# Performance work log

Measured on AMD Instinct MI355X. Metric: run time of the kernel, lower is better.

## Reference

```python
import jax, jax.numpy as jnp
import numpy as np

N_NODES = 100000
N_EDGES = 1600000
IN_F = 256
OUT_F = 64


def setup_inputs() -> dict:
    key = jax.random.key(0)
    k1, k2, k3, k4, k5, k6 = jax.random.split(key, 6)
    x = jax.random.normal(k1, (N_NODES, IN_F), dtype=jnp.float32)
    edge_vals = jax.random.uniform(k2, (N_EDGES,), dtype=jnp.float32)
    W = jax.random.normal(k3, (IN_F, OUT_F), dtype=jnp.float32) * (1.0 / np.sqrt(OUT_F))
    bias = jax.random.normal(k4, (OUT_F,), dtype=jnp.float32) * (1.0 / np.sqrt(OUT_F))
    row_idx = jnp.sort(jax.random.randint(k5, (N_EDGES,), 0, N_NODES, dtype=jnp.int32))
    col_idx = jax.random.randint(k6, (N_EDGES,), 0, N_NODES, dtype=jnp.int32)
    return {"x": x, "edge_vals": edge_vals, "W": W, "bias": bias,
            "row_idx": row_idx, "col_idx": col_idx}


def reference(x, edge_vals, W, bias, row_idx, col_idx):
    # support = X @ W  (dense GEMM; torch.mm / torch.spmm branch)
    support = x @ W                                  # [N, OUT_F]
    # flexspmm: output = A @ support, A given as weighted edge list
    msgs = support[col_idx] * edge_vals[:, None]      # [E, OUT_F] gather + scale
    out = jax.ops.segment_sum(msgs, row_idx, num_segments=x.shape[0])  # [N, OUT_F]
    return out + bias
```

## Files before the change

### kernel.cpp

```cpp
#include <hip/hip_runtime.h>
#include <hip/hip_bf16.h>

#define N_NODES 100000
#define N_EDGES 1600000
#define IN_F 256
#define OUT_F 64

typedef short bf16x8 __attribute__((ext_vector_type(8)));
typedef float f32x4 __attribute__((ext_vector_type(4)));
typedef unsigned short u16x8 __attribute__((ext_vector_type(8)));

__device__ __forceinline__ short f2bf(float f) {
  unsigned u = __float_as_uint(f);
  u += 0x7FFF + ((u >> 16) & 1);
  return (short)(u >> 16);
}
__device__ __forceinline__ float bf2f(unsigned short u) {
  return __uint_as_float(((unsigned)u) << 16);
}

__global__ __launch_bounds__(256) void prep_kernel(
    const int* __restrict__ row_idx, int* __restrict__ row_ptr,
    const float* __restrict__ W, short* __restrict__ Wf) {
  const int b = blockIdx.x;
  if (b < 392) {
    int i = b * 256 + threadIdx.x;
    if (i > N_NODES) return;
    int lo = 0, hi = N_EDGES;
    while (lo < hi) {
      int mid = (lo + hi) >> 1;
      if (row_idx[mid] < i) lo = mid + 1; else hi = mid;
    }
    row_ptr[i] = lo;
  } else {
    int tid = (b - 392) * 256 + threadIdx.x;
    int s = tid >> 8;
    int r = tid & 255;
    int t = r >> 6;
    int lane = r & 63;
    int col = t * 16 + (lane & 15);
    int kbase = s * 32 + ((lane >> 4) & 3) * 8;
#pragma unroll
    for (int j = 0; j < 8; ++j) {
      Wf[(size_t)tid * 8 + j] = f2bf(W[(size_t)(kbase + j) * OUT_F + col]);
    }
  }
}

__global__ __launch_bounds__(256) void gemm_kernel(
    const float* __restrict__ x, const short* __restrict__ Wf,
    unsigned short* __restrict__ supB) {
  __shared__ short sWf[8 * 4 * 64 * 8];
  {
    const float4* g = reinterpret_cast<const float4*>(Wf);
    float4* s4 = reinterpret_cast<float4*>(sWf);
#pragma unroll
    for (int i = 0; i < 8; ++i) s4[threadIdx.x + i * 256] = g[threadIdx.x + i * 256];
  }
  __syncthreads();

  const int lane = threadIdx.x & 63;
  const int wave = threadIdx.x >> 6;
  const int r0_base = blockIdx.x * 64 + wave * 16;

  int arow = r0_base + (lane & 15);
  if (arow >= N_NODES) arow = N_NODES - 1;
  const float* xrow = x + (size_t)arow * IN_F + ((lane >> 4) & 3) * 8;

  f32x4 acc0 = {0.f, 0.f, 0.f, 0.f};
  f32x4 acc1 = {0.f, 0.f, 0.f, 0.f};
  f32x4 acc2 = {0.f, 0.f, 0.f, 0.f};
  f32x4 acc3 = {0.f, 0.f, 0.f, 0.f};

#pragma unroll
  for (int s = 0; s < 8; ++s) {
    const float4 f0 = *reinterpret_cast<const float4*>(xrow + s * 32);
    const float4 f1 = *reinterpret_cast<const float4*>(xrow + s * 32 + 4);
    bf16x8 a;
    a[0] = f2bf(f0.x); a[1] = f2bf(f0.y); a[2] = f2bf(f0.z); a[3] = f2bf(f0.w);
    a[4] = f2bf(f1.x); a[5] = f2bf(f1.y); a[6] = f2bf(f1.z); a[7] = f2bf(f1.w);
    const bf16x8 b0 = *reinterpret_cast<const bf16x8*>(&sWf[((s * 4 + 0) * 64 + lane) * 8]);
    const bf16x8 b1 = *reinterpret_cast<const bf16x8*>(&sWf[((s * 4 + 1) * 64 + lane) * 8]);
    const bf16x8 b2 = *reinterpret_cast<const bf16x8*>(&sWf[((s * 4 + 2) * 64 + lane) * 8]);
    const bf16x8 b3 = *reinterpret_cast<const bf16x8*>(&sWf[((s * 4 + 3) * 64 + lane) * 8]);
    acc0 = __builtin_amdgcn_mfma_f32_16x16x32_bf16(a, b0, acc0, 0, 0, 0);
    acc1 = __builtin_amdgcn_mfma_f32_16x16x32_bf16(a, b1, acc1, 0, 0, 0);
    acc2 = __builtin_amdgcn_mfma_f32_16x16x32_bf16(a, b2, acc2, 0, 0, 0);
    acc3 = __builtin_amdgcn_mfma_f32_16x16x32_bf16(a, b3, acc3, 0, 0, 0);
  }

  const int orow_base = r0_base + ((lane >> 4) & 3) * 4;
  const int ocol = lane & 15;
#pragma unroll
  for (int r = 0; r < 4; ++r) {
    const int row = orow_base + r;
    if (row < N_NODES) {
      unsigned short* o = supB + (size_t)row * OUT_F + ocol;
      o[0]  = (unsigned short)f2bf(acc0[r]);
      o[16] = (unsigned short)f2bf(acc1[r]);
      o[32] = (unsigned short)f2bf(acc2[r]);
      o[48] = (unsigned short)f2bf(acc3[r]);
    }
  }
}

__global__ __launch_bounds__(256) void spmm_kernel(
    const unsigned short* __restrict__ supB, const float* __restrict__ ev,
    const int* __restrict__ col, const int* __restrict__ row_ptr,
    const float* __restrict__ bias, float* __restrict__ out) {
  const int lane = threadIdx.x & 63;
  const int g = lane >> 3;
  const int fo = lane & 7;
  const int gwave = (blockIdx.x * blockDim.x + threadIdx.x) >> 6;
  const int nwaves = (gridDim.x * blockDim.x) >> 6;

  const int per = (N_NODES + nwaves - 1) / nwaves;
  const int n0 = gwave * per;
  if (n0 >= N_NODES) return;
  const int n1 = (n0 + per < N_NODES) ? n0 + per : N_NODES;

  float b[8];
#pragma unroll
  for (int j = 0; j < 8; ++j) b[j] = bias[fo * 8 + j];

  int n = n0;
  int i = row_ptr[n0];
  int eCur = row_ptr[n0 + 1];
  int eNext = row_ptr[(n0 + 2 <= N_NODES) ? n0 + 2 : N_NODES];

  int pos0 = i + g, pos1 = i + 8 + g;
  int cp0 = pos0 < N_EDGES ? pos0 : N_EDGES - 1;
  int cp1 = pos1 < N_EDGES ? pos1 : N_EDGES - 1;
  int   c0 = col[cp0];
  int   c1 = col[cp1];
  float v0 = ev[cp0];
  float v1 = ev[cp1];

  float acc[8] = {0.f, 0.f, 0.f, 0.f, 0.f, 0.f, 0.f, 0.f};

  while (true) {
    const bool more = (i + 16 < eCur);
    const int ni = more ? (i + 16) : eCur;

    const int np0 = ni + g, np1 = ni + 8 + g;
    const int ncp0 = np0 < N_EDGES ? np0 : N_EDGES - 1;
    const int ncp1 = np1 < N_EDGES ? np1 : N_EDGES - 1;
    const int   nc0 = col[ncp0];
    const int   nc1 = col[ncp1];
    const float nv0 = ev[ncp0];
    const float nv1 = ev[ncp1];

    const float u0 = (pos0 < eCur) ? v0 : 0.f;
    const float u1 = (pos1 < eCur) ? v1 : 0.f;
    const u16x8 s0 = *reinterpret_cast<const u16x8*>(supB + (size_t)c0 * OUT_F + fo * 8);
    const u16x8 s1 = *reinterpret_cast<const u16x8*>(supB + (size_t)c1 * OUT_F + fo * 8);
#pragma unroll
    for (int j = 0; j < 8; ++j) acc[j] = fmaf(u0, bf2f(s0[j]), acc[j]);
#pragma unroll
    for (int j = 0; j < 8; ++j) acc[j] = fmaf(u1, bf2f(s1[j]), acc[j]);

    if (!more) {
#pragma unroll
      for (int j = 0; j < 8; ++j) {
        acc[j] += __shfl_xor(acc[j], 8);
        acc[j] += __shfl_xor(acc[j], 16);
        acc[j] += __shfl_xor(acc[j], 32);
      }
      if (lane < 8) {
        float* o = out + (size_t)n * OUT_F + fo * 8;
        f32x4 oA = {acc[0] + b[0], acc[1] + b[1], acc[2] + b[2], acc[3] + b[3]};
        f32x4 oB = {acc[4] + b[4], acc[5] + b[5], acc[6] + b[6], acc[7] + b[7]};
        *reinterpret_cast<f32x4*>(o) = oA;
        *reinterpret_cast<f32x4*>(o + 4) = oB;
      }
      ++n;
      if (n >= n1) break;
#pragma unroll
      for (int j = 0; j < 8; ++j) acc[j] = 0.f;
      eCur = eNext;
      eNext = row_ptr[(n + 2 <= N_NODES) ? n + 2 : N_NODES];
    }

    i = ni;
    pos0 = np0; pos1 = np1;
    c0 = nc0; c1 = nc1;
    v0 = nv0; v1 = nv1;
  }
}

extern "C" void kernel_launch(void* const* d_in, const int* in_sizes, int n_in,
                              void* d_out, int out_size, void* d_ws, size_t ws_size,
                              hipStream_t stream) {
  const float* x        = (const float*)d_in[0];
  const float* ev       = (const float*)d_in[1];
  const float* W        = (const float*)d_in[2];
  const float* bias     = (const float*)d_in[3];
  const int*   row_idx  = (const int*)d_in[4];
  const int*   col_idx  = (const int*)d_in[5];
  float* out = (float*)d_out;

  int*            row_ptr = (int*)d_ws;
  short*          Wf      = (short*)((char*)d_ws + 448 * 1024);
  unsigned short* supB    = (unsigned short*)((char*)d_ws + 512 * 1024);

  prep_kernel<<<400, 256, 0, stream>>>(row_idx, row_ptr, W, Wf);

  gemm_kernel<<<(N_NODES + 63) / 64, 256, 0, stream>>>(x, Wf, supB);

  spmm_kernel<<<2048, 256, 0, stream>>>(supB, ev, col_idx, row_ptr, bias, out);
}
```

Measured before the change: 70.20 us.

## Balance SpMM waves by edge count and store support in fp16

Each SpMM wave now gets an equal share of edges, with row boundaries found from the sorted row_idx, instead of an equal share of nodes. This is meant to reduce tail imbalance between waves. The intermediate support matrix is stored as fp16 instead of bf16, which uses hardware half-to-float conversion in the gather loop and narrower 32-bit address arithmetic. The fp16 storage risks overflow or precision differences, and rows that straddle a partition boundary are assigned to a single wave.

```diff
diff --git a/kernel.cpp b/kernel.cpp
--- a/kernel.cpp
+++ b/kernel.cpp
@@ -1,5 +1,6 @@
 #include <hip/hip_runtime.h>
 #include <hip/hip_bf16.h>
+#include <hip/hip_fp16.h>
 
 #define N_NODES 100000
 #define N_EDGES 1600000
@@ -8,15 +9,12 @@
 
 typedef short bf16x8 __attribute__((ext_vector_type(8)));
 typedef float f32x4 __attribute__((ext_vector_type(4)));
-typedef unsigned short u16x8 __attribute__((ext_vector_type(8)));
+typedef _Float16 half8 __attribute__((ext_vector_type(8)));
 
 __device__ __forceinline__ short f2bf(float f) {
   unsigned u = __float_as_uint(f);
   u += 0x7FFF + ((u >> 16) & 1);
   return (short)(u >> 16);
-}
-__device__ __forceinline__ float bf2f(unsigned short u) {
-  return __uint_as_float(((unsigned)u) << 16);
 }
 
 __global__ __launch_bounds__(256) void prep_kernel(
@@ -49,7 +47,7 @@
 
 __global__ __launch_bounds__(256) void gemm_kernel(
     const float* __restrict__ x, const short* __restrict__ Wf,
-    unsigned short* __restrict__ supB) {
+    _Float16* __restrict__ supH) {
   __shared__ short sWf[8 * 4 * 64 * 8];
   {
     const float4* g = reinterpret_cast<const float4*>(Wf);
@@ -95,18 +93,19 @@
   for (int r = 0; r < 4; ++r) {
     const int row = orow_base + r;
     if (row < N_NODES) {
-      unsigned short* o = supB + (size_t)row * OUT_F + ocol;
-      o[0]  = (unsigned short)f2bf(acc0[r]);
-      o[16] = (unsigned short)f2bf(acc1[r]);
-      o[32] = (unsigned short)f2bf(acc2[r]);
-      o[48] = (unsigned short)f2bf(acc3[r]);
+      _Float16* o = supH + (size_t)row * OUT_F + ocol;
+      o[0]  = (_Float16)acc0[r];
+      o[16] = (_Float16)acc1[r];
+      o[32] = (_Float16)acc2[r];
+      o[48] = (_Float16)acc3[r];
     }
   }
 }
 
 __global__ __launch_bounds__(256) void spmm_kernel(
-    const unsigned short* __restrict__ supB, const float* __restrict__ ev,
+    const _Float16* __restrict__ supH, const float* __restrict__ ev,
     const int* __restrict__ col, const int* __restrict__ row_ptr,
+    const int* __restrict__ row_idx,
     const float* __restrict__ bias, float* __restrict__ out) {
   const int lane = threadIdx.x & 63;
   const int g = lane >> 3;
@@ -114,10 +113,11 @@
   const int gwave = (blockIdx.x * blockDim.x + threadIdx.x) >> 6;
   const int nwaves = (gridDim.x * blockDim.x) >> 6;
 
-  const int per = (N_NODES + nwaves - 1) / nwaves;
-  const int n0 = gwave * per;
-  if (n0 >= N_NODES) return;
-  const int n1 = (n0 + per < N_NODES) ? n0 + per : N_NODES;
+  const long k0 = ((long)gwave * N_EDGES) / nwaves;
+  const long k1 = ((long)(gwave + 1) * N_EDGES) / nwaves;
+  const int n0 = (k0 == 0) ? 0 : (row_idx[k0 - 1] + 1);
+  const int n1 = (gwave + 1 >= nwaves) ? N_NODES : (row_idx[k1 - 1] + 1);
+  if (n0 >= n1) return;
 
   float b[8];
 #pragma unroll
@@ -152,12 +152,14 @@
 
     const float u0 = (pos0 < eCur) ? v0 : 0.f;
     const float u1 = (pos1 < eCur) ? v1 : 0.f;
-    const u16x8 s0 = *reinterpret_cast<const u16x8*>(supB + (size_t)c0 * OUT_F + fo * 8);
-    const u16x8 s1 = *reinterpret_cast<const u16x8*>(supB + (size_t)c1 * OUT_F + fo * 8);
-#pragma unroll
-    for (int j = 0; j < 8; ++j) acc[j] = fmaf(u0, bf2f(s0[j]), acc[j]);
-#pragma unroll
-    for (int j = 0; j < 8; ++j) acc[j] = fmaf(u1, bf2f(s1[j]), acc[j]);
+    const half8 s0 = *reinterpret_cast<const half8*>(
+        supH + (unsigned)((c0 << 6) + fo * 8));
+    const half8 s1 = *reinterpret_cast<const half8*>(
+        supH + (unsigned)((c1 << 6) + fo * 8));
+#pragma unroll
+    for (int j = 0; j < 8; ++j) acc[j] = fmaf(u0, (float)s0[j], acc[j]);
+#pragma unroll
+    for (int j = 0; j < 8; ++j) acc[j] = fmaf(u1, (float)s1[j], acc[j]);
 
     if (!more) {
 #pragma unroll
@@ -199,13 +201,13 @@
   const int*   col_idx  = (const int*)d_in[5];
   float* out = (float*)d_out;
 
-  int*            row_ptr = (int*)d_ws;
-  short*          Wf      = (short*)((char*)d_ws + 448 * 1024);
-  unsigned short* supB    = (unsigned short*)((char*)d_ws + 512 * 1024);
+  int*       row_ptr = (int*)d_ws;
+  short*     Wf      = (short*)((char*)d_ws + 448 * 1024);
+  _Float16*  supH    = (_Float16*)((char*)d_ws + 512 * 1024);
 
   prep_kernel<<<400, 256, 0, stream>>>(row_idx, row_ptr, W, Wf);
 
-  gemm_kernel<<<(N_NODES + 63) / 64, 256, 0, stream>>>(x, Wf, supB);
-
-  spmm_kernel<<<2048, 256, 0, stream>>>(supB, ev, col_idx, row_ptr, bias, out);
-}
+  gemm_kernel<<<(N_NODES + 63) / 64, 256, 0, stream>>>(x, Wf, supH);
+
+  spmm_kernel<<<2048, 256, 0, stream>>>(supH, ev, col_idx, row_ptr, row_idx, bias, out);
+}
```

Result: no change. 69.26 us, median of 2 (-1.3%).
